# Performance work log

Hardware: AMD Instinct MI355X
Metric: run time of the kernel (lower is better)

The kernel has to match this reference:

```python
import jax, jax.numpy as jnp
import numpy as np

EMBED_DIM = 512
NUM_HEADS = 16
WIN = (8, 8)
N_TOK = WIN[0] * WIN[1]           # 64 tokens per window
HEAD_DIM = EMBED_DIM // NUM_HEADS  # 32
SCALE = HEAD_DIM ** -0.5
B_WIN = 1024                       # batch * num_windows
NUM_WINDOWS = 256                  # windows per image -> batch images = 4


def _relative_bias_index(window_size):
    wh, ww = window_size
    coords = np.stack(np.meshgrid(np.arange(wh), np.arange(ww), indexing='ij'))  # (2, wh, ww)
    flat = coords.reshape(2, -1)                                   # (2, N)
    rel = (flat[:, :, None] - flat[:, None, :]).transpose(1, 2, 0)  # (N, N, 2)
    rel[:, :, 0] += wh - 1
    rel[:, :, 1] += ww - 1
    rel[:, :, 0] *= 2 * ww - 1
    return rel.sum(-1)  # (N, N) int


def setup_inputs() -> dict:
    key = jax.random.key(0)
    ks = jax.random.split(key, 6)
    x = jax.random.normal(ks[0], (B_WIN, N_TOK, EMBED_DIM), dtype=jnp.float32)
    attention_mask = jax.random.normal(ks[1], (NUM_WINDOWS, N_TOK, N_TOK), dtype=jnp.float32)
    qkv_w = jax.random.normal(ks[2], (EMBED_DIM, 3 * EMBED_DIM), dtype=jnp.float32) * 0.02
    qkv_b = jnp.zeros((3 * EMBED_DIM,), dtype=jnp.float32)
    proj_w = jax.random.normal(ks[3], (EMBED_DIM, EMBED_DIM), dtype=jnp.float32) * 0.02
    proj_b = jnp.zeros((EMBED_DIM,), dtype=jnp.float32)
    n_bias = (2 * WIN[0] - 1) * (2 * WIN[1] - 1)  # 225
    bias_table = jax.random.normal(ks[4], (n_bias, NUM_HEADS), dtype=jnp.float32) * 0.02
    rel_index = jnp.asarray(_relative_bias_index(WIN), dtype=jnp.int32)  # (N, N)
    return {"x": x, "attention_mask": attention_mask, "qkv_w": qkv_w, "qkv_b": qkv_b,
            "proj_w": proj_w, "proj_b": proj_b, "bias_table": bias_table, "rel_index": rel_index}


def reference(x, attention_mask, qkv_w, qkv_b, proj_w, proj_b, bias_table, rel_index):
    B, N, C = x.shape
    nw = attention_mask.shape[0]
    bimg = B // nw
    qkv = x @ qkv_w + qkv_b                              # (B, N, 3C)
    # original rearrange 'b n (h d c) -> d b n h c' groups last dim as (heads, 3, head_dim)
    qkv = qkv.reshape(B, N, NUM_HEADS, 3, HEAD_DIM)
    q, k, v = qkv[..., 0, :], qkv[..., 1, :], qkv[..., 2, :]  # each (B, N, H, hd)
    attn = jnp.einsum('bqhd,bkhd->bhqk', q, k) * SCALE        # (B, H, N, N)
    bias = bias_table[rel_index].transpose(2, 0, 1)           # (H, N, N)
    attn = attn + bias[None]
    attn = attn.reshape(bimg, nw, NUM_HEADS, N, N) + attention_mask[None, :, None]
    attn = jax.nn.softmax(attn, axis=-1).reshape(B, NUM_HEADS, N, N)
    out = jnp.einsum('bhqk,bkhd->bqhd', attn, v).reshape(B, N, C)
    return out @ proj_w + proj_b
```

## Files before the change

kernel.cpp:

```cpp
#include <hip/hip_runtime.h>
#include <hip/hip_bf16.h>


typedef unsigned short u16;
typedef __bf16 bx8 __attribute__((ext_vector_type(8)));
typedef float f4_t __attribute__((ext_vector_type(4)));

#define QKV_ELEMS 33554432ull
#define SCALE 0.17677669529663687f

static __device__ __forceinline__ u16 f2b(float f) {
    return __builtin_bit_cast(u16, (__bf16)f);
}

typedef const unsigned int __attribute__((address_space(1)))* gas_t;
typedef unsigned int __attribute__((address_space(3)))* las_t;
static __device__ __forceinline__ void glds16(const void* g, void* l) {
    __builtin_amdgcn_global_load_lds((gas_t)g, (las_t)l, 16, 0, 0);
}

__global__ void cvt_k(const float* __restrict__ X, u16* __restrict__ Xb) {
    size_t i = ((size_t)blockIdx.x * 256 + threadIdx.x) * 8;
    float4 v0 = *(const float4*)(X + i);
    float4 v1 = *(const float4*)(X + i + 4);
    ushort4 p0, p1;
    p0.x = f2b(v0.x); p0.y = f2b(v0.y); p0.z = f2b(v0.z); p0.w = f2b(v0.w);
    p1.x = f2b(v1.x); p1.y = f2b(v1.y); p1.z = f2b(v1.z); p1.w = f2b(v1.w);
    *(ushort4*)(Xb + i) = p0;
    *(ushort4*)(Xb + i + 4) = p1;
}

__global__ void wt_k(const float* __restrict__ W, u16* __restrict__ Wt,
                     int K, int N) {
    int idx = blockIdx.x * 256 + threadIdx.x;
    if (idx >= N * K) return;
    int n = idx / K, k = idx - n * K;
    Wt[idx] = f2b(W[(size_t)k * N + n]);
}

__global__ void bias_k(const float* __restrict__ bias_table,
                       const int* __restrict__ rel_index,
                       float* __restrict__ bias_full) {
    int idx = blockIdx.x * 256 + threadIdx.x;
    int h = idx >> 12, rc = idx & 4095;
    bias_full[idx] = bias_table[rel_index[rc] * 16 + h];
}


#define MF(av, mt)                                                            \
    acc[mt][0] = __builtin_amdgcn_mfma_f32_16x16x32_bf16(av, b0, acc[mt][0],  \
                                                         0, 0, 0);            \
    acc[mt][1] = __builtin_amdgcn_mfma_f32_16x16x32_bf16(av, b1, acc[mt][1],  \
                                                         0, 0, 0);            \
    acc[mt][2] = __builtin_amdgcn_mfma_f32_16x16x32_bf16(av, b2, acc[mt][2],  \
                                                         0, 0, 0);            \
    acc[mt][3] = __builtin_amdgcn_mfma_f32_16x16x32_bf16(av, b3, acc[mt][3],  \
                                                         0, 0, 0);

#define TILE_STEP(T, DOSTAGE, VMC)                                            \
    {                                                                         \
        const char* aT = ldsA + ((T) & 3) * 16384 + wm * 8192 + foff;         \
        const char* bT = ldsB + ((T) & 3) * 16384 + wn * 4096 + foff;         \
        bx8 b0 = *(const bx8*)(bT);                                           \
        bx8 b1 = *(const bx8*)(bT + 1024);                                    \
        bx8 b2 = *(const bx8*)(bT + 2048);                                    \
        bx8 b3 = *(const bx8*)(bT + 3072);                                    \
        bx8 a0 = *(const bx8*)(aT);                                           \
        bx8 a1 = *(const bx8*)(aT + 1024);                                    \
        bx8 a2 = *(const bx8*)(aT + 2048);                                    \
        bx8 a3 = *(const bx8*)(aT + 3072);                                    \
        if (DOSTAGE) STAGE_A((T) + 3);                                        \
        __builtin_amdgcn_s_barrier();                                         \
        __builtin_amdgcn_s_setprio(1);                                        \
        MF(a0, 0) MF(a1, 1) MF(a2, 2) MF(a3, 3)                               \
        __builtin_amdgcn_s_setprio(0);                                        \
        __builtin_amdgcn_s_barrier();                                         \
        bx8 a4 = *(const bx8*)(aT + 4096);                                    \
        bx8 a5 = *(const bx8*)(aT + 5120);                                    \
        bx8 a6 = *(const bx8*)(aT + 6144);                                    \
        bx8 a7 = *(const bx8*)(aT + 7168);                                    \
        if (DOSTAGE) STAGE_B((T) + 3);                                        \
        if ((VMC) == 8) asm volatile("s_waitcnt vmcnt(8)" ::: "memory");      \
        else if ((VMC) == 4) asm volatile("s_waitcnt vmcnt(4)" ::: "memory"); \
        else if ((VMC) == 0) asm volatile("s_waitcnt vmcnt(0)" ::: "memory"); \
        __builtin_amdgcn_s_barrier();                                         \
        __builtin_amdgcn_s_setprio(1);                                        \
        MF(a4, 4) MF(a5, 5) MF(a6, 6) MF(a7, 7)                               \
        __builtin_amdgcn_s_setprio(0);                                        \
        __builtin_amdgcn_s_barrier();                                         \
    }

template <int MODE>
__global__ __launch_bounds__(512, 2) void gemm256_k(
    const u16* __restrict__ A, const u16* __restrict__ Bt,
    const float* __restrict__ bias, void* __restrict__ Out) {
    extern __shared__ __align__(16) char smem[];
    const int tid = threadIdx.x;
    const int wave = tid >> 6, lane = tid & 63;
    const int l16 = lane & 15, quad = lane >> 4;
    const int wm = wave >> 2, wn = wave & 3;

    const int NT_COL = (MODE == 0) ? 6 : 2;
    const int NWG = (MODE == 0) ? 1536 : 512;
    const int bid = blockIdx.x;
    const int swz = (bid & 7) * (NWG >> 3) + (bid >> 3);
    const int m0 = (swz / NT_COL) << 8;
    const int n0 = (swz % NT_COL) << 8;

    char* const ldsA = smem;
    char* const ldsB = smem + 65536;

    const int lr = lane >> 2, lc = lane & 3;
    const int swzc = (lc ^ ((lr >> 1) & 3)) * 8;
    const int stoff = wave * 1024;

    const u16* Asrc0;
    const u16* Asrc1;
    if (MODE == 0) {
        const int r0 = m0 + wave * 16 + lr;
        Asrc0 = A + (size_t)r0 * 512 + swzc;
        Asrc1 = Asrc0 + (size_t)128 * 512;
    } else {
        const int r0 = m0 + wave * 16 + lr, r1 = r0 + 128;
        Asrc0 = A + (size_t)(r0 >> 6) * 2048 + (r0 & 63) * 32 + swzc;
        Asrc1 = A + (size_t)(r1 >> 6) * 2048 + (r1 & 63) * 32 + swzc;
    }
    const u16* Bsrc0 = Bt + (size_t)(n0 + wave * 16 + lr) * 512 + swzc;
    const u16* Bsrc1 = Bsrc0 + (size_t)128 * 512;

    auto STAGE_A = [&](int T) {
        char* d = ldsA + (T & 3) * 16384 + stoff;
        if (MODE == 0) {
            glds16(Asrc0 + T * 32, d);
            glds16(Asrc1 + T * 32, d + 8192);
        } else {
            glds16(Asrc0 + (size_t)T * 2097152, d);
            glds16(Asrc1 + (size_t)T * 2097152, d + 8192);
        }
    };
    auto STAGE_B = [&](int T) {
        char* d = ldsB + (T & 3) * 16384 + stoff;
        glds16(Bsrc0 + T * 32, d);
        glds16(Bsrc1 + T * 32, d + 8192);
    };

    const int foff = l16 * 64 + ((quad ^ ((l16 >> 1) & 3)) * 16);

    f4_t acc[8][4];
#pragma unroll
    for (int i = 0; i < 8; ++i)
#pragma unroll
        for (int j = 0; j < 4; ++j) acc[i][j] = (f4_t){0.f, 0.f, 0.f, 0.f};

    STAGE_A(0); STAGE_B(0); STAGE_A(1); STAGE_B(1); STAGE_A(2); STAGE_B(2);
    asm volatile("s_waitcnt vmcnt(8)" ::: "memory");
    __builtin_amdgcn_s_barrier();

    for (int T = 0; T < 13; ++T) TILE_STEP(T, true, 8);
    TILE_STEP(13, false, 4);
    TILE_STEP(14, false, 0);
    TILE_STEP(15, false, -1);

    float bv[4];
#pragma unroll
    for (int nt = 0; nt < 4; ++nt) bv[nt] = bias[n0 + wn * 64 + nt * 16 + l16];

    if (MODE == 0) {
        u16* c_s = (u16*)smem;
        u16* qkvp = (u16*)Out;
        const int cg = n0 + wave * 32;
        const int hh = cg / 96;
        const int which = (cg - hh * 96) >> 5;
        u16* plane = qkvp + (size_t)which * QKV_ELEMS + (size_t)hh * 2048;
#pragma unroll
        for (int p = 0; p < 2; ++p) {
            if (wm == p) {
#pragma unroll
                for (int mt = 0; mt < 8; ++mt)
#pragma unroll
                    for (int nt = 0; nt < 4; ++nt)
#pragma unroll
                        for (int i = 0; i < 4; ++i)
                            c_s[(mt * 16 + quad * 4 + i) * 264 +
                                wn * 64 + nt * 16 + l16] =
                                f2b(acc[mt][nt][i] + bv[nt]);
            }
            __syncthreads();
#pragma unroll
            for (int j = 0; j < 8; ++j) {
                int row = j * 16 + (lane >> 2);
                int gm = m0 + p * 128 + row;
                int w_win = gm >> 6, tok = gm & 63;
                uint4 v = *(const uint4*)&c_s[row * 264 + wave * 32 +
                                              (lane & 3) * 8];
                *(uint4*)(plane + (size_t)w_win * 32768 + tok * 32 +
                          (lane & 3) * 8) = v;
            }
            __syncthreads();
        }
    } else {
        float* c_sf = (float*)smem;
        float* Of = (float*)Out;
#pragma unroll
        for (int p = 0; p < 4; ++p) {
            if (wm == (p >> 1)) {
                const int mtb = (p & 1) * 4;
#pragma unroll
                for (int mt2 = 0; mt2 < 4; ++mt2)
#pragma unroll
                    for (int nt = 0; nt < 4; ++nt)
#pragma unroll
                        for (int i = 0; i < 4; ++i)
                            c_sf[(mt2 * 16 + quad * 4 + i) * 264 +
                                 wn * 64 + nt * 16 + l16] =
                                acc[mtb + mt2][nt][i] + bv[nt];
            }
            __syncthreads();
#pragma unroll
            for (int j = 0; j < 8; ++j) {
                int flat = tid + 512 * j;
                int r = flat >> 6, c4 = (flat & 63) * 4;
                float4 v = *(const float4*)&c_sf[r * 264 + c4];
                *(float4*)&Of[(size_t)(m0 + p * 64 + r) * 512 + n0 + c4] = v;
            }
            __syncthreads();
        }
    }
}

__global__ __launch_bounds__(256) void attn_k(
    const u16* __restrict__ qkv, const float* __restrict__ mask,
    const float* __restrict__ biasf, u16* __restrict__ attn_out) {
    const int bx = blockIdx.x;
    const int w = bx >> 4, h = bx & 15;
    const int wmk = w & 255;
    const int tid = threadIdx.x;
    const int wave = tid >> 6, lane = tid & 63;
    const int quad = lane >> 4, l16 = lane & 15;

    __shared__ alignas(16) u16 q_s[64 * 40];
    __shared__ alignas(16) u16 k_s[64 * 40];
    __shared__ alignas(16) u16 vT[32 * 72];
    __shared__ alignas(16) float s_s[64 * 68];
    __shared__ alignas(16) u16 p_s[64 * 72];

    const size_t base = (size_t)((w << 4) + h) * 2048;
    {
        int tok = tid >> 2, d0 = (tid & 3) * 8;
        uint4 qv = *(const uint4*)(qkv + base + tid * 8);
        *(uint4*)&q_s[tok * 40 + d0] = qv;
        uint4 kv = *(const uint4*)(qkv + QKV_ELEMS + base + tid * 8);
        *(uint4*)&k_s[tok * 40 + d0] = kv;
        uint4 vv = *(const uint4*)(qkv + 2 * QKV_ELEMS + base + tid * 8);
        const u16* pv = (const u16*)&vv;
#pragma unroll
        for (int j = 0; j < 8; ++j) vT[(d0 + j) * 72 + tok] = pv[j];
    }
    __syncthreads();

    {
        bx8 a = *(const bx8*)&q_s[(wave * 16 + l16) * 40 + quad * 8];
#pragma unroll
        for (int nt = 0; nt < 4; ++nt) {
            bx8 b = *(const bx8*)&k_s[(nt * 16 + l16) * 40 + quad * 8];
            f4_t acc = (f4_t){0.f, 0.f, 0.f, 0.f};
            acc = __builtin_amdgcn_mfma_f32_16x16x32_bf16(a, b, acc, 0, 0, 0);
#pragma unroll
            for (int i = 0; i < 4; ++i) {
                int r = wave * 16 + quad * 4 + i;
                int c = nt * 16 + l16;
                float s = acc[i] * SCALE + biasf[(h << 12) + (r << 6) + c] +
                          mask[((size_t)wmk * 64 + r) * 64 + c];
                s_s[r * 68 + c] = s;
            }
        }
    }
    __syncthreads();

    {
        int row = tid >> 2, j = (tid & 3) * 16;
        float mx = -1e30f;
#pragma unroll
        for (int cc = 0; cc < 16; ++cc) mx = fmaxf(mx, s_s[row * 68 + j + cc]);
        mx = fmaxf(mx, __shfl_xor(mx, 1));
        mx = fmaxf(mx, __shfl_xor(mx, 2));
        float e[16], sum = 0.f;
#pragma unroll
        for (int cc = 0; cc < 16; ++cc) {
            e[cc] = __expf(s_s[row * 68 + j + cc] - mx);
            sum += e[cc];
        }
        sum += __shfl_xor(sum, 1);
        sum += __shfl_xor(sum, 2);
        float inv = 1.f / sum;
#pragma unroll
        for (int cc = 0; cc < 16; ++cc) p_s[row * 72 + j + cc] = f2b(e[cc] * inv);
    }
    __syncthreads();

    {
        u16* os = (u16*)s_s;
#pragma unroll
        for (int nt = 0; nt < 2; ++nt) {
            f4_t acc = (f4_t){0.f, 0.f, 0.f, 0.f};
#pragma unroll
            for (int ks = 0; ks < 2; ++ks) {
                bx8 a = *(const bx8*)&p_s[(wave * 16 + l16) * 72 + ks * 32 + quad * 8];
                bx8 b = *(const bx8*)&vT[(nt * 16 + l16) * 72 + ks * 32 + quad * 8];
                acc = __builtin_amdgcn_mfma_f32_16x16x32_bf16(a, b, acc, 0, 0, 0);
            }
#pragma unroll
            for (int i = 0; i < 4; ++i)
                os[(wave * 16 + quad * 4 + i) * 40 + nt * 16 + l16] =
                    f2b(acc[i]);
        }
        __syncthreads();
        int tok = tid >> 2, d8 = (tid & 3) * 8;
        uint4 v = *(const uint4*)&os[tok * 40 + d8];
        *(uint4*)(attn_out + ((((size_t)h << 10) + w) << 11) + tid * 8) = v;
    }
}

extern "C" void kernel_launch(void* const* d_in, const int* in_sizes, int n_in,
                              void* d_out, int out_size, void* d_ws,
                              size_t ws_size, hipStream_t stream) {
    const float* x      = (const float*)d_in[0];
    const float* mask   = (const float*)d_in[1];
    const float* qkv_w  = (const float*)d_in[2];
    const float* qkv_b  = (const float*)d_in[3];
    const float* proj_w = (const float*)d_in[4];
    const float* proj_b = (const float*)d_in[5];
    const float* bias_t = (const float*)d_in[6];
    const int*   rel    = (const int*)d_in[7];
    float* out = (float*)d_out;

    char* ws = (char*)d_ws;
    u16* Wt1 = (u16*)ws;      ws += (size_t)1536 * 512 * 2;
    u16* Wt2 = (u16*)ws;      ws += (size_t)512 * 512 * 2;
    float* biasf = (float*)ws; ws += (size_t)16 * 64 * 64 * 4;
    u16* qkv = (u16*)ws;      ws += 3 * QKV_ELEMS * 2;
    u16* attn = (u16*)ws;     ws += QKV_ELEMS * 2;
    u16* xb = attn;

    cvt_k<<<16384, 256, 0, stream>>>(x, xb);
    wt_k<<<3072, 256, 0, stream>>>(qkv_w, Wt1, 512, 1536);
    wt_k<<<1024, 256, 0, stream>>>(proj_w, Wt2, 512, 512);
    bias_k<<<256, 256, 0, stream>>>(bias_t, rel, biasf);
    gemm256_k<0><<<1536, 512, 131072, stream>>>(xb, Wt1, qkv_b, qkv);
    attn_k<<<16384, 256, 0, stream>>>(qkv, mask, biasf, attn);
    gemm256_k<1><<<512, 512, 131072, stream>>>(attn, Wt2, proj_b, out);
}
```

Baseline: 483.7 us.

## Software-pipeline LDS fragment reads across GEMM phases with register double-buffering

Restructures the GEMM main loop into even and odd phases. Each phase issues the LDS reads for the next half-tile or next tile (A low/high halves and double-buffered B fragments) before running the MFMAs on data already in registers, with explicit lgkmcnt waits and sched_barriers. It also drops two of the four barriers per tile, so LDS read latency overlaps with MFMA work. The cost is more live vector registers and hand-tuned vmcnt/lgkmcnt counts that must exactly match the staging pattern.

After: 496.4 us. 1.03x slower.

```diff
diff --git a/kernel.cpp b/kernel.cpp
--- a/kernel.cpp
+++ b/kernel.cpp
@@ -47,47 +47,56 @@
 }
 
 
-#define MF(av, mt)                                                            \
-    acc[mt][0] = __builtin_amdgcn_mfma_f32_16x16x32_bf16(av, b0, acc[mt][0],  \
-                                                         0, 0, 0);            \
-    acc[mt][1] = __builtin_amdgcn_mfma_f32_16x16x32_bf16(av, b1, acc[mt][1],  \
-                                                         0, 0, 0);            \
-    acc[mt][2] = __builtin_amdgcn_mfma_f32_16x16x32_bf16(av, b2, acc[mt][2],  \
-                                                         0, 0, 0);            \
-    acc[mt][3] = __builtin_amdgcn_mfma_f32_16x16x32_bf16(av, b3, acc[mt][3],  \
-                                                         0, 0, 0);
-
-#define TILE_STEP(T, DOSTAGE, VMC)                                            \
+#define MF1(av, bv, mt, nt)                                                   \
+    acc[mt][nt] = __builtin_amdgcn_mfma_f32_16x16x32_bf16(av, bv,             \
+                                                          acc[mt][nt], 0, 0, 0);
+#define MF4(av, mt, B)                                                        \
+    MF1(av, B[0], mt, 0) MF1(av, B[1], mt, 1)                                 \
+    MF1(av, B[2], mt, 2) MF1(av, B[3], mt, 3)
+
+#define PH_EVEN(T, DOST, BCUR)                                                \
     {                                                                         \
+        asm volatile("s_barrier" ::: "memory");                               \
         const char* aT = ldsA + ((T) & 3) * 16384 + wm * 8192 + foff;         \
-        const char* bT = ldsB + ((T) & 3) * 16384 + wn * 4096 + foff;         \
-        bx8 b0 = *(const bx8*)(bT);                                           \
-        bx8 b1 = *(const bx8*)(bT + 1024);                                    \
-        bx8 b2 = *(const bx8*)(bT + 2048);                                    \
-        bx8 b3 = *(const bx8*)(bT + 3072);                                    \
-        bx8 a0 = *(const bx8*)(aT);                                           \
-        bx8 a1 = *(const bx8*)(aT + 1024);                                    \
-        bx8 a2 = *(const bx8*)(aT + 2048);                                    \
-        bx8 a3 = *(const bx8*)(aT + 3072);                                    \
-        if (DOSTAGE) STAGE_A((T) + 3);                                        \
-        __builtin_amdgcn_s_barrier();                                         \
+        aHi[0] = *(const bx8*)(aT + 4096);                                    \
+        aHi[1] = *(const bx8*)(aT + 5120);                                    \
+        aHi[2] = *(const bx8*)(aT + 6144);                                    \
+        aHi[3] = *(const bx8*)(aT + 7168);                                    \
+        if (DOST) STAGE_A((T) + 3);                                           \
+        asm volatile("s_waitcnt lgkmcnt(4)" ::: "memory");                    \
+        __builtin_amdgcn_sched_barrier(0);                                    \
         __builtin_amdgcn_s_setprio(1);                                        \
-        MF(a0, 0) MF(a1, 1) MF(a2, 2) MF(a3, 3)                               \
+        MF4(aLo[0], 0, BCUR) MF4(aLo[1], 1, BCUR)                             \
+        MF4(aLo[2], 2, BCUR) MF4(aLo[3], 3, BCUR)                             \
         __builtin_amdgcn_s_setprio(0);                                        \
-        __builtin_amdgcn_s_barrier();                                         \
-        bx8 a4 = *(const bx8*)(aT + 4096);                                    \
-        bx8 a5 = *(const bx8*)(aT + 5120);                                    \
-        bx8 a6 = *(const bx8*)(aT + 6144);                                    \
-        bx8 a7 = *(const bx8*)(aT + 7168);                                    \
-        if (DOSTAGE) STAGE_B((T) + 3);                                        \
-        if ((VMC) == 8) asm volatile("s_waitcnt vmcnt(8)" ::: "memory");      \
+    }
+
+#define PH_ODD(T, DOST, VMC, DORD, BCUR, BNXT)                                \
+    {                                                                         \
+        if ((VMC) == 6) asm volatile("s_waitcnt vmcnt(6)" ::: "memory");      \
         else if ((VMC) == 4) asm volatile("s_waitcnt vmcnt(4)" ::: "memory"); \
         else if ((VMC) == 0) asm volatile("s_waitcnt vmcnt(0)" ::: "memory"); \
-        __builtin_amdgcn_s_barrier();                                         \
+        asm volatile("s_barrier" ::: "memory");                               \
+        if (DORD) {                                                           \
+            const char* aN = ldsA + (((T) + 1) & 3) * 16384 + wm * 8192 + foff;\
+            const char* bN = ldsB + (((T) + 1) & 3) * 16384 + wn * 4096 + foff;\
+            BNXT[0] = *(const bx8*)(bN);                                      \
+            BNXT[1] = *(const bx8*)(bN + 1024);                               \
+            BNXT[2] = *(const bx8*)(bN + 2048);                               \
+            BNXT[3] = *(const bx8*)(bN + 3072);                               \
+            aLo[0] = *(const bx8*)(aN);                                       \
+            aLo[1] = *(const bx8*)(aN + 1024);                                \
+            aLo[2] = *(const bx8*)(aN + 2048);                                \
+            aLo[3] = *(const bx8*)(aN + 3072);                                \
+        }                                                                     \
+        if (DOST) STAGE_B((T) + 3);                                           \
+        if (DORD) asm volatile("s_waitcnt lgkmcnt(8)" ::: "memory");          \
+        else      asm volatile("s_waitcnt lgkmcnt(0)" ::: "memory");          \
+        __builtin_amdgcn_sched_barrier(0);                                    \
         __builtin_amdgcn_s_setprio(1);                                        \
-        MF(a4, 4) MF(a5, 5) MF(a6, 6) MF(a7, 7)                               \
+        MF4(aHi[0], 4, BCUR) MF4(aHi[1], 5, BCUR)                             \
+        MF4(aHi[2], 6, BCUR) MF4(aHi[3], 7, BCUR)                             \
         __builtin_amdgcn_s_setprio(0);                                        \
-        __builtin_amdgcn_s_barrier();                                         \
     }
 
 template <int MODE>
@@ -152,14 +161,42 @@
 #pragma unroll
         for (int j = 0; j < 4; ++j) acc[i][j] = (f4_t){0.f, 0.f, 0.f, 0.f};
 
+    bx8 aLo[4], aHi[4], bA[4], bB[4];
+
     STAGE_A(0); STAGE_B(0); STAGE_A(1); STAGE_B(1); STAGE_A(2); STAGE_B(2);
     asm volatile("s_waitcnt vmcnt(8)" ::: "memory");
-    __builtin_amdgcn_s_barrier();
-
-    for (int T = 0; T < 13; ++T) TILE_STEP(T, true, 8);
-    TILE_STEP(13, false, 4);
-    TILE_STEP(14, false, 0);
-    TILE_STEP(15, false, -1);
+    asm volatile("s_barrier" ::: "memory");
+    {
+        const char* aT = ldsA + wm * 8192 + foff;
+        const char* bT = ldsB + wn * 4096 + foff;
+        bA[0] = *(const bx8*)(bT);
+        bA[1] = *(const bx8*)(bT + 1024);
+        bA[2] = *(const bx8*)(bT + 2048);
+        bA[3] = *(const bx8*)(bT + 3072);
+        aLo[0] = *(const bx8*)(aT);
+        aLo[1] = *(const bx8*)(aT + 1024);
+        aLo[2] = *(const bx8*)(aT + 2048);
+        aLo[3] = *(const bx8*)(aT + 3072);
+    }
+
+    PH_EVEN(0, 1, bA)  PH_ODD(0, 1, 6, 1, bA, bB)
+    PH_EVEN(1, 1, bB)  PH_ODD(1, 1, 6, 1, bB, bA)
+    PH_EVEN(2, 1, bA)  PH_ODD(2, 1, 6, 1, bA, bB)
+    PH_EVEN(3, 1, bB)  PH_ODD(3, 1, 6, 1, bB, bA)
+    PH_EVEN(4, 1, bA)  PH_ODD(4, 1, 6, 1, bA, bB)
+    PH_EVEN(5, 1, bB)  PH_ODD(5, 1, 6, 1, bB, bA)
+    PH_EVEN(6, 1, bA)  PH_ODD(6, 1, 6, 1, bA, bB)
+    PH_EVEN(7, 1, bB)  PH_ODD(7, 1, 6, 1, bB, bA)
+    PH_EVEN(8, 1, bA)  PH_ODD(8, 1, 6, 1, bA, bB)
+    PH_EVEN(9, 1, bB)  PH_ODD(9, 1, 6, 1, bB, bA)
+    PH_EVEN(10, 1, bA) PH_ODD(10, 1, 6, 1, bA, bB)
+    PH_EVEN(11, 1, bB) PH_ODD(11, 1, 6, 1, bB, bA)
+    PH_EVEN(12, 1, bA) PH_ODD(12, 1, 6, 1, bA, bB)
+    PH_EVEN(13, 0, bB) PH_ODD(13, 0, 4, 1, bB, bA)
+    PH_EVEN(14, 0, bA) PH_ODD(14, 0, 0, 1, bA, bB)
+    PH_EVEN(15, 0, bB) PH_ODD(15, 0, -1, 0, bB, bA)
+
+    __syncthreads();
 
     float bv[4];
 #pragma unroll
```
